# Kernel tuning notes

Measured on AMD Instinct MI355X. Metric: run time of the kernel, lower is better.

The kernel has to match this reference:

```python
import jax, jax.numpy as jnp
import numpy as np

# dims: N nodes, E edges, C channel multiplicity, NS species, RB radial basis, H radial mlp hidden
N, E, C, NS, RB, H = 4000, 128000, 128, 5, 8, 64
AVG_N = 32.0  # avg_n_neighbors


def setup_inputs() -> dict:
    key = jax.random.key(0)
    ks = jax.random.split(key, 17)
    return {
        "x_scalars": jax.random.normal(ks[0], (N, C), jnp.float32),
        "x_vectors": jax.random.normal(ks[1], (N, C, 3), jnp.float32),
        "edge_vectors": jax.random.normal(ks[2], (E, 3), jnp.float32) * 2.0,
        "radial_basis": jax.random.normal(ks[3], (E, RB), jnp.float32),
        "W1_0": jax.random.normal(ks[4], (C, C), jnp.float32),
        "W1_1": jax.random.normal(ks[5], (C, C), jnp.float32),
        "rmlp_w0": jax.random.normal(ks[6], (RB, H), jnp.float32) * np.float32(np.sqrt(4.0 / RB)),
        "rmlp_w1": jax.random.normal(ks[7], (H, H), jnp.float32) * np.float32(np.sqrt(4.0 / H)),
        "rmlp_w2": jax.random.normal(ks[8], (H, H), jnp.float32) * np.float32(np.sqrt(4.0 / H)),
        "rmlp_w3": jax.random.normal(ks[9], (H, 4 * C), jnp.float32) * np.float32(np.sqrt(1.0 / H)),
        "W2_0": jax.random.normal(ks[10], (2 * C, 2 * C), jnp.float32),
        "W2_1": jax.random.normal(ks[11], (2 * C, C), jnp.float32),
        "Wsk0": jax.random.normal(ks[12], (NS, C, 2 * C), jnp.float32),
        "Wsk1": jax.random.normal(ks[13], (NS, C, C), jnp.float32),
        "species": jax.random.randint(ks[14], (N,), 0, NS),
        "senders": jax.random.randint(ks[15], (E,), 0, N),
        "receivers": jax.random.randint(ks[16], (E,), 0, N),
    }


def reference(x_scalars, x_vectors, edge_vectors, radial_basis,
              W1_0, W1_1, rmlp_w0, rmlp_w1, rmlp_w2, rmlp_w3,
              W2_0, W2_1, Wsk0, Wsk1, species, senders, receivers):
    n_nodes = x_scalars.shape[0]
    inv_c = 1.0 / jnp.sqrt(jnp.float32(C))
    # linear_1: per-irrep channel mixing (e3nn path-normalized Linear)
    y0 = (x_scalars @ W1_0) * inv_c                                  # [N,C] 0e
    y1 = jnp.einsum('nci,cd->ndi', x_vectors, W1_1) * inv_c          # [N,C,3] 1o
    # gather to edges
    m0 = y0[senders]                                                 # [E,C]
    m1 = y1[senders]                                                 # [E,C,3]
    # spherical harmonics lmax=1, component normalization: Y0=1, Y1=sqrt(3)*unit_vec
    r = jnp.linalg.norm(edge_vectors, axis=1, keepdims=True)
    u = edge_vectors / jnp.maximum(r, 1e-12)
    Y1 = jnp.sqrt(3.0) * u                                           # [E,3]
    # tensor product filtered to 0e,1o (explicit Clebsch-Gordan, component norm)
    t0a = m0                                                         # 0e x 0e -> 0e
    t0b = jnp.einsum('eci,ei->ec', m1, Y1) / jnp.sqrt(3.0)           # 1o x 1o -> 0e
    t1a = m0[:, :, None] * Y1[:, None, :]                            # 0e x 1o -> 1o
    t1b = m1                                                         # 1o x 0e -> 1o
    # radial MLP (silu, no bias), one scalar weight per tp irrep (4C total)
    h = jax.nn.silu(radial_basis @ rmlp_w0)
    h = jax.nn.silu(h @ rmlp_w1)
    h = jax.nn.silu(h @ rmlp_w2)
    w = h @ rmlp_w3                                                  # [E,4C]
    ws0, ws1 = w[:, :C], w[:, C:2 * C]
    wv0, wv1 = w[:, 2 * C:3 * C], w[:, 3 * C:]
    scal = jnp.concatenate([t0a * ws0, t0b * ws1], axis=1)           # [E,2C]
    vec = jnp.concatenate([t1a * wv0[:, :, None], t1b * wv1[:, :, None]], axis=1)  # [E,2C,3]
    # scatter-add to receivers, neighbor normalization
    inv_nb = 1.0 / jnp.sqrt(jnp.float32(AVG_N))
    agg_s = jax.ops.segment_sum(scal, receivers, num_segments=n_nodes) * inv_nb
    agg_v = jax.ops.segment_sum(vec, receivers, num_segments=n_nodes) * inv_nb
    # linear_2: tp irreps -> (2C)x0e + Cx1o  (C output scalars + C gates)
    inv_2c = 1.0 / jnp.sqrt(jnp.float32(2 * C))
    s = (agg_s @ W2_0) * inv_2c                                      # [N,2C]
    v = jnp.einsum('nci,cd->ndi', agg_v, W2_1) * inv_2c              # [N,C,3]
    # indexed (per-species) skip connection
    s = s + jnp.einsum('nc,ncd->nd', x_scalars, Wsk0[species]) * inv_c
    v = v + jnp.einsum('nci,ncd->ndi', x_vectors, Wsk1[species]) * inv_c
    # gate: silu on scalars, silu(gates) multiplies 1o features
    out_s = jax.nn.silu(s[:, :C])
    gates = jax.nn.silu(s[:, C:])
    out_v = v * gates[:, :, None]
    return jnp.concatenate([out_s, out_v.reshape(n_nodes, 3 * C)], axis=1)  # [N,4C]
```

## Files before the change

kernel.cpp:

```cpp
#include <hip/hip_runtime.h>
#include <math.h>

#define CC 128
#define HH 64
#define RBD 8
#define WDIM 512

typedef __attribute__((ext_vector_type(8))) short short8v;
typedef __attribute__((ext_vector_type(4))) float f32x4;

__device__ __forceinline__ float silu_f(float x) {
    return x / (1.0f + __expf(-x));
}

__device__ __forceinline__ unsigned short f2bf(float x) {
    unsigned int b = __float_as_uint(x);
    unsigned int r = (b + 0x7FFFu + ((b >> 16) & 1u)) >> 16;
    return (unsigned short)r;
}

__device__ __forceinline__ float bf2f(unsigned short u) {
    return __uint_as_float(((unsigned int)u) << 16);
}

__global__ void k_prep(const float* __restrict__ w0, const float* __restrict__ w1,
                       const float* __restrict__ w2, const float* __restrict__ w3,
                       float* __restrict__ w0T, float* __restrict__ w1T,
                       float* __restrict__ w2T, float* __restrict__ w3T,
                       unsigned short* __restrict__ w3bs,
                       unsigned short* __restrict__ w0b,
                       unsigned short* __restrict__ w1b,
                       unsigned short* __restrict__ w2b) {
    int i = blockIdx.x * blockDim.x + threadIdx.x;
    if (i < 64 * 8) { int m = i / 8, k = i % 8; w0T[i] = w0[k * 64 + m]; }
    if (i < 64 * 64) { int m = i / 64, k = i % 64; w1T[i] = w1[k * 64 + m]; w2T[i] = w2[k * 64 + m]; }
    if (i < 512 * 64) { int j = i / 64, k = i % 64; w3T[i] = w3[k * 512 + j]; }
    if (i < 32768) {
        int t = i >> 10, ch = (i >> 9) & 1, lane = (i >> 3) & 63, j = i & 7;
        int k = ch * 32 + 8 * (lane >> 4) + j;
        int n = t * 16 + (lane & 15);
        w3bs[i] = f2bf(w3[k * 512 + n]);
    }
    if (i < 2048) {
        int t = i >> 9, lane = (i >> 3) & 63, j = i & 7;
        int k = 8 * (lane >> 4) + j;
        int col = t * 16 + (lane & 15);
        w0b[i] = (k < RBD) ? f2bf(w0[k * 64 + col]) : (unsigned short)0;
    }
    if (i < 4096) {
        int f = i >> 9, lane = (i >> 3) & 63, j = i & 7;
        int ks = f >> 2, t = f & 3;
        int k = ks * 32 + 8 * (lane >> 4) + j;
        int col = t * 16 + (lane & 15);
        w1b[i] = f2bf(w1[k * 64 + col]);
        w2b[i] = f2bf(w2[k * 64 + col]);
    }
}

__global__ void k_hist(const int* __restrict__ rcv, int* __restrict__ deg, int E_,
                       const int* __restrict__ species, int* __restrict__ scnt, int N) {
    int e = blockIdx.x * blockDim.x + threadIdx.x;
    if (e < E_) atomicAdd(&deg[rcv[e]], 1);
    if (e < N) atomicAdd(&scnt[species[e]], 1);
}

__global__ __launch_bounds__(1024) void k_scan(const int* __restrict__ deg,
                                               int* __restrict__ off, int N,
                                               const int* __restrict__ scnt,
                                               int* __restrict__ soff, int NS) {
    __shared__ int s[1024];
    int t = threadIdx.x;
    int b = t * 4;
    int a0 = (b + 0 < N) ? deg[b + 0] : 0;
    int a1 = (b + 1 < N) ? deg[b + 1] : 0;
    int a2 = (b + 2 < N) ? deg[b + 2] : 0;
    int a3 = (b + 3 < N) ? deg[b + 3] : 0;
    int part = a0 + a1 + a2 + a3;
    s[t] = part;
    __syncthreads();
    for (int d = 1; d < 1024; d <<= 1) {
        int v = (t >= d) ? s[t - d] : 0;
        __syncthreads();
        s[t] += v;
        __syncthreads();
    }
    int excl = s[t] - part;
    if (b + 0 <= N) off[b + 0] = excl;
    if (b + 1 <= N) off[b + 1] = excl + a0;
    if (b + 2 <= N) off[b + 2] = excl + a0 + a1;
    if (b + 3 <= N) off[b + 3] = excl + a0 + a1 + a2;
    if (t == 0) {
        int acc = 0;
        for (int q = 0; q < NS; q++) { soff[q] = acc; acc += scnt[q]; }
        soff[NS] = acc;
    }
}

__global__ void k_scatter(const int* __restrict__ rcv, const int* __restrict__ off,
                          int* __restrict__ cur, int* __restrict__ elist, int E_,
                          const int* __restrict__ species, const int* __restrict__ soff,
                          int* __restrict__ scur, int* __restrict__ nlist, int N) {
    int e = blockIdx.x * blockDim.x + threadIdx.x;
    if (e < E_) {
        int r = rcv[e];
        int p = atomicAdd(&cur[r], 1);
        elist[off[r] + p] = e;
    }
    if (e < N) {
        int s = species[e];
        int p = atomicAdd(&scur[s], 1);
        nlist[soff[s] + p] = e;
    }
}

__global__ __launch_bounds__(128) void k_node_lin(
    const float* __restrict__ xs, const float* __restrict__ xv,
    const float* __restrict__ W10, const float* __restrict__ W11,
    float* __restrict__ y0, float* __restrict__ y1, int N) {
    const int d = threadIdx.x;
    const int n0 = blockIdx.x * 2;
    const int NP = N * CC;
    const float inv_c = 0.08838834764831845f;
    float a0[2] = {0.f, 0.f};
    float av[2][3] = {};
    #pragma unroll 4
    for (int c = 0; c < CC; c++) {
        float w10 = W10[c * CC + d];
        float w11 = W11[c * CC + d];
        #pragma unroll
        for (int n = 0; n < 2; n++) {
            a0[n] += xs[(n0 + n) * CC + c] * w10;
            #pragma unroll
            for (int i = 0; i < 3; i++)
                av[n][i] += xv[((n0 + n) * CC + c) * 3 + i] * w11;
        }
    }
    #pragma unroll
    for (int n = 0; n < 2; n++) {
        y0[(n0 + n) * CC + d] = a0[n] * inv_c;
        #pragma unroll
        for (int i = 0; i < 3; i++)
            y1[i * NP + (n0 + n) * CC + d] = av[n][i] * inv_c;
    }
}

__device__ __forceinline__ void layer64(const float4* a, float4* b,
                                        const float* __restrict__ W) {
    #pragma unroll
    for (int m = 0; m < 16; m++) {
        float s0 = 0.f, s1 = 0.f, s2 = 0.f, s3 = 0.f;
        const float* w0p = W + (4 * m + 0) * 64;
        const float* w1p = W + (4 * m + 1) * 64;
        const float* w2p = W + (4 * m + 2) * 64;
        const float* w3p = W + (4 * m + 3) * 64;
        #pragma unroll
        for (int k = 0; k < 16; k++) {
            float4 av = a[k];
            s0 += av.x * w0p[4 * k + 0] + av.y * w0p[4 * k + 1] + av.z * w0p[4 * k + 2] + av.w * w0p[4 * k + 3];
            s1 += av.x * w1p[4 * k + 0] + av.y * w1p[4 * k + 1] + av.z * w1p[4 * k + 2] + av.w * w1p[4 * k + 3];
            s2 += av.x * w2p[4 * k + 0] + av.y * w2p[4 * k + 1] + av.z * w2p[4 * k + 2] + av.w * w2p[4 * k + 3];
            s3 += av.x * w3p[4 * k + 0] + av.y * w3p[4 * k + 1] + av.z * w3p[4 * k + 2] + av.w * w3p[4 * k + 3];
        }
        b[m] = make_float4(silu_f(s0), silu_f(s1), silu_f(s2), silu_f(s3));
    }
}

__device__ __forceinline__ void mlp_body(
    const float* __restrict__ rb, int e,
    const float* __restrict__ w0T, const float* __restrict__ w1T,
    const float* __restrict__ w2T, float4* a) {
    float rbv[RBD];
    #pragma unroll
    for (int k = 0; k < RBD; k++) rbv[k] = rb[(size_t)e * RBD + k];
    float4 b[16];
    #pragma unroll
    for (int m = 0; m < 16; m++) {
        float s0 = 0.f, s1 = 0.f, s2 = 0.f, s3 = 0.f;
        #pragma unroll
        for (int k = 0; k < RBD; k++) {
            float rv = rbv[k];
            s0 += rv * w0T[(4 * m + 0) * RBD + k];
            s1 += rv * w0T[(4 * m + 1) * RBD + k];
            s2 += rv * w0T[(4 * m + 2) * RBD + k];
            s3 += rv * w0T[(4 * m + 3) * RBD + k];
        }
        a[m] = make_float4(silu_f(s0), silu_f(s1), silu_f(s2), silu_f(s3));
    }
    layer64(a, b, w1T);
    layer64(b, a, w2T);
}

__global__ __launch_bounds__(256) void k_mlpw3(
    const float* __restrict__ rb, const int* __restrict__ elist,
    const int* __restrict__ snd, const float* __restrict__ evec,
    const unsigned short* __restrict__ w0b, const unsigned short* __restrict__ w1b,
    const unsigned short* __restrict__ w2b, const unsigned short* __restrict__ w3bs,
    unsigned int* __restrict__ Wq, float4* __restrict__ up, int* __restrict__ sp,
    int E_) {
    const int lane = threadIdx.x & 63;
    const int wv = threadIdx.x >> 6;
    const int rbk = blockIdx.x * 4 + wv;
    const int col = lane & 15;
    const int grp = lane >> 4;

    if (threadIdx.x < 64) {
        int p = blockIdx.x * 64 + threadIdx.x;
        if (p < E_) {
            int e = elist[p];
            float e0 = evec[(size_t)e * 3 + 0];
            float e1 = evec[(size_t)e * 3 + 1];
            float e2 = evec[(size_t)e * 3 + 2];
            float rn = sqrtf(e0 * e0 + e1 * e1 + e2 * e2);
            float inv = 1.0f / fmaxf(rn, 1e-12f);
            up[p] = make_float4(e0 * inv, e1 * inv, e2 * inv, 0.f);
            sp[p] = snd[e];
        }
    }

    __shared__ unsigned short hbuf[4][16][72];

    short8v a0 = (short8v){0, 0, 0, 0, 0, 0, 0, 0};
    if (grp == 0) {
        int e = elist[rbk * 16 + col];
        const float* rp = rb + (size_t)e * RBD;
        #pragma unroll
        for (int j = 0; j < RBD; j++) a0[j] = (short)f2bf(rp[j]);
    }
    f32x4 acc[4];
    {
        const unsigned short* bp = w0b + (size_t)lane * 8;
        #pragma unroll
        for (int t = 0; t < 4; t++) {
            short8v b = *(const short8v*)(bp + (size_t)t * 512);
            acc[t] = __builtin_amdgcn_mfma_f32_16x16x32_bf16(
                a0, b, (f32x4){0.f, 0.f, 0.f, 0.f}, 0, 0, 0);
        }
    }
    #pragma unroll
    for (int t = 0; t < 4; t++)
        #pragma unroll
        for (int r = 0; r < 4; r++)
            hbuf[wv][grp * 4 + r][t * 16 + col] = f2bf(silu_f(acc[t][r]));

    {
        short8v aA = *(const short8v*)&hbuf[wv][col][8 * grp];
        short8v aB = *(const short8v*)&hbuf[wv][col][32 + 8 * grp];
        const unsigned short* bp = w1b + (size_t)lane * 8;
        #pragma unroll
        for (int t = 0; t < 4; t++) {
            short8v b0 = *(const short8v*)(bp + (size_t)(0 + t) * 512);
            short8v b1 = *(const short8v*)(bp + (size_t)(4 + t) * 512);
            f32x4 c = __builtin_amdgcn_mfma_f32_16x16x32_bf16(
                aA, b0, (f32x4){0.f, 0.f, 0.f, 0.f}, 0, 0, 0);
            acc[t] = __builtin_amdgcn_mfma_f32_16x16x32_bf16(aB, b1, c, 0, 0, 0);
        }
    }
    #pragma unroll
    for (int t = 0; t < 4; t++)
        #pragma unroll
        for (int r = 0; r < 4; r++)
            hbuf[wv][grp * 4 + r][t * 16 + col] = f2bf(silu_f(acc[t][r]));

    {
        short8v aA = *(const short8v*)&hbuf[wv][col][8 * grp];
        short8v aB = *(const short8v*)&hbuf[wv][col][32 + 8 * grp];
        const unsigned short* bp = w2b + (size_t)lane * 8;
        #pragma unroll
        for (int t = 0; t < 4; t++) {
            short8v b0 = *(const short8v*)(bp + (size_t)(0 + t) * 512);
            short8v b1 = *(const short8v*)(bp + (size_t)(4 + t) * 512);
            f32x4 c = __builtin_amdgcn_mfma_f32_16x16x32_bf16(
                aA, b0, (f32x4){0.f, 0.f, 0.f, 0.f}, 0, 0, 0);
            acc[t] = __builtin_amdgcn_mfma_f32_16x16x32_bf16(aB, b1, c, 0, 0, 0);
        }
    }
    #pragma unroll
    for (int t = 0; t < 4; t++)
        #pragma unroll
        for (int r = 0; r < 4; r++)
            hbuf[wv][grp * 4 + r][t * 16 + col] = f2bf(silu_f(acc[t][r]));

    short8v A0 = *(const short8v*)&hbuf[wv][col][8 * grp];
    short8v A1 = *(const short8v*)&hbuf[wv][col][32 + 8 * grp];

    f32x4 wacc[32];
    #pragma unroll
    for (int t = 0; t < 32; t++) wacc[t] = (f32x4){0.f, 0.f, 0.f, 0.f};

    const unsigned short* bbase = w3bs + (size_t)lane * 8;
    #pragma unroll
    for (int t = 0; t < 32; t++) {
        short8v b0 = *(const short8v*)(bbase + (size_t)(t * 2 + 0) * 512);
        short8v b1 = *(const short8v*)(bbase + (size_t)(t * 2 + 1) * 512);
        wacc[t] = __builtin_amdgcn_mfma_f32_16x16x32_bf16(A0, b0, wacc[t], 0, 0, 0);
        wacc[t] = __builtin_amdgcn_mfma_f32_16x16x32_bf16(A1, b1, wacc[t], 0, 0, 0);
    }

    const int rowq = grp * 4;
    const int jbase = rbk * 16 + rowq;
    #pragma unroll
    for (int t = 0; t < 16; t++) {
        #pragma unroll
        for (int rr = 0; rr < 4; rr++) {
            unsigned lo = f2bf(wacc[t][rr]);
            unsigned hi = f2bf(wacc[t + 16][rr]);
            Wq[(size_t)(jbase + rr) * 256 + t * 16 + col] = lo | (hi << 16);
        }
    }
}

__global__ __launch_bounds__(256, 4) void k_gather_em(
    const int* __restrict__ off, const float4* __restrict__ up,
    const int* __restrict__ sp, const unsigned int* __restrict__ Wq,
    const float* __restrict__ y0, const float* __restrict__ y1, int NP,
    float* __restrict__ agg_s, float* __restrict__ agg_v) {
    const int r = blockIdx.x;
    const int tid = threadIdx.x;
    const int half = tid >> 7;
    const int c = tid & 127;
    const int start = off[r];
    const int end = off[r + 1];

    float accs = 0.f, av0 = 0.f, av1 = 0.f, av2 = 0.f;
    const float SQ3 = 1.7320508075688772f;

    auto proc = [&](unsigned wq, float4 u, int s) {
        float wa = bf2f((unsigned short)(wq & 0xFFFFu));
        float wb = bf2f((unsigned short)(wq >> 16));
        if (half == 0) {
            float f = y0[(size_t)s * CC + c];
            accs += f * wa;
            float bb = f * wb * SQ3;
            av0 += bb * u.x; av1 += bb * u.y; av2 += bb * u.z;
        } else {
            float f0 = y1[0 * NP + s * CC + c];
            float f1 = y1[1 * NP + s * CC + c];
            float f2 = y1[2 * NP + s * CC + c];
            accs += (f0 * u.x + f1 * u.y + f2 * u.z) * wa;
            av0 += f0 * wb; av1 += f1 * wb; av2 += f2 * wb;
        }
    };

    int j = start;
    for (; j + 4 <= end; j += 4) {
        unsigned wq0 = Wq[(size_t)(j + 0) * 256 + tid];
        unsigned wq1 = Wq[(size_t)(j + 1) * 256 + tid];
        unsigned wq2 = Wq[(size_t)(j + 2) * 256 + tid];
        unsigned wq3 = Wq[(size_t)(j + 3) * 256 + tid];
        float4 u0 = up[j + 0], u1 = up[j + 1], u2 = up[j + 2], u3 = up[j + 3];
        int s0 = __builtin_amdgcn_readfirstlane(sp[j + 0]);
        int s1 = __builtin_amdgcn_readfirstlane(sp[j + 1]);
        int s2 = __builtin_amdgcn_readfirstlane(sp[j + 2]);
        int s3 = __builtin_amdgcn_readfirstlane(sp[j + 3]);
        proc(wq0, u0, s0);
        proc(wq1, u1, s1);
        proc(wq2, u2, s2);
        proc(wq3, u3, s3);
    }
    for (; j < end; j++) {
        unsigned wq = Wq[(size_t)j * 256 + tid];
        float4 u = up[j];
        int s = __builtin_amdgcn_readfirstlane(sp[j]);
        proc(wq, u, s);
    }

    agg_s[(size_t)r * 256 + tid] = accs;
    float* o = agg_v + ((size_t)r * 256 + tid) * 3;
    o[0] = av0; o[1] = av1; o[2] = av2;
}

__global__ __launch_bounds__(256) void k_mlp_wp(
    const float* __restrict__ rb, const int* __restrict__ elist,
    const float* __restrict__ w0T, const float* __restrict__ w1T,
    const float* __restrict__ w2T, const float* __restrict__ w3T,
    unsigned short* __restrict__ Wp, int E_) {
    int p = blockIdx.x * blockDim.x + threadIdx.x;
    if (p >= E_) return;
    int e = elist[p];
    const int c0 = blockIdx.y * 128;

    float4 a[16];
    mlp_body(rb, e, w0T, w1T, w2T, a);

    const size_t E4 = (size_t)E_ * 4;
    for (int c = c0; c < c0 + 128; c += 8) {
        float s[8];
        #pragma unroll
        for (int q = 0; q < 8; q++) {
            const float* rp = w3T + (size_t)(c + q) * 64;
            float t0 = 0.f, t1 = 0.f, t2 = 0.f, t3 = 0.f;
            #pragma unroll
            for (int k = 0; k < 16; k++) {
                float4 h = a[k];
                t0 += h.x * rp[4 * k + 0];
                t1 += h.y * rp[4 * k + 1];
                t2 += h.z * rp[4 * k + 2];
                t3 += h.w * rp[4 * k + 3];
            }
            s[q] = (t0 + t1) + (t2 + t3);
        }
        ushort4 pk0 = make_ushort4(f2bf(s[0]), f2bf(s[1]), f2bf(s[2]), f2bf(s[3]));
        ushort4 pk1 = make_ushort4(f2bf(s[4]), f2bf(s[5]), f2bf(s[6]), f2bf(s[7]));
        *(ushort4*)(Wp + (size_t)(c >> 2) * E4 + (size_t)p * 4) = pk0;
        *(ushort4*)(Wp + (size_t)((c >> 2) + 1) * E4 + (size_t)p * 4) = pk1;
    }
}

__global__ __launch_bounds__(512, 2) void k_gather_wg(
    const int* __restrict__ off, const int* __restrict__ elist,
    const int* __restrict__ snd, const float* __restrict__ evec,
    const unsigned short* __restrict__ Wp, int E_,
    const float* __restrict__ y0, const float* __restrict__ y1, int NP,
    float* __restrict__ agg_s, float* __restrict__ agg_v) {
    const int r = blockIdx.x;
    const int tid = threadIdx.x;
    const int part = tid >> 7;
    const int c = tid & 127;

    const int start = off[r];
    const int end = off[r + 1];

    const unsigned short* __restrict__ wstream =
        Wp + (size_t)(tid >> 2) * ((size_t)E_ * 4) + (tid & 3);

    float acc0 = 0.f, acc1 = 0.f, acc2 = 0.f;
    const float SQ3 = 1.7320508075688772f;

    #pragma unroll 2
    for (int j = start; j < end; j++) {
        int e = elist[j];
        e = __builtin_amdgcn_readfirstlane(e);
        int s = snd[e];
        s = __builtin_amdgcn_readfirstlane(s);

        float e0 = evec[(size_t)e * 3 + 0];
        float e1 = evec[(size_t)e * 3 + 1];
        float e2 = evec[(size_t)e * 3 + 2];
        float rn = sqrtf(e0 * e0 + e1 * e1 + e2 * e2);
        float inv = 1.0f / fmaxf(rn, 1e-12f);
        float ux = e0 * inv, uy = e1 * inv, uz = e2 * inv;

        float w = bf2f(wstream[(size_t)j * 4]);

        if (part == 0) {
            acc0 += y0[(size_t)s * CC + c] * w;
        } else if (part == 1) {
            float f = y1[0 * NP + s * CC + c] * ux
                    + y1[1 * NP + s * CC + c] * uy
                    + y1[2 * NP + s * CC + c] * uz;
            acc0 += f * w;
        } else if (part == 2) {
            float bb = y0[(size_t)s * CC + c] * w * SQ3;
            acc0 += bb * ux; acc1 += bb * uy; acc2 += bb * uz;
        } else {
            acc0 += y1[0 * NP + s * CC + c] * w;
            acc1 += y1[1 * NP + s * CC + c] * w;
            acc2 += y1[2 * NP + s * CC + c] * w;
        }
    }

    if (part == 0) {
        agg_s[(size_t)r * 256 + c] = acc0;
    } else if (part == 1) {
        agg_s[(size_t)r * 256 + 128 + c] = acc0;
    } else if (part == 2) {
        float* o = agg_v + ((size_t)r * 256 + c) * 3;
        o[0] = acc0; o[1] = acc1; o[2] = acc2;
    } else {
        float* o = agg_v + ((size_t)r * 256 + 128 + c) * 3;
        o[0] = acc0; o[1] = acc1; o[2] = acc2;
    }
}

__global__ void k_mlp(const float* __restrict__ rb,
                      const float* __restrict__ w0T, const float* __restrict__ w1T,
                      const float* __restrict__ w2T,
                      float* __restrict__ h2, int E_) {
    int e = blockIdx.x * blockDim.x + threadIdx.x;
    if (e >= E_) return;
    float4 a[16];
    mlp_body(rb, e, w0T, w1T, w2T, a);
    float4* out = (float4*)(h2 + (size_t)e * HH);
    #pragma unroll
    for (int q = 0; q < 16; q++) out[q] = a[q];
}

__global__ __launch_bounds__(512, 1) void k_gather_h2(
    const int* __restrict__ off, const int* __restrict__ elist,
    const int* __restrict__ snd, const float* __restrict__ evec,
    const float* __restrict__ h2, const float* __restrict__ w3T,
    const float* __restrict__ y0, const float* __restrict__ y1, int NP,
    float* __restrict__ agg_s, float* __restrict__ agg_v) {
    const int r = blockIdx.x;
    const int tid = threadIdx.x;
    const int part = tid >> 7;
    const int c = tid & 127;

    const float4* wp = (const float4*)(w3T + (size_t)tid * 64);
    const int start = off[r];
    const int end = off[r + 1];

    float acc0 = 0.f, acc1 = 0.f, acc2 = 0.f;
    const float SQ3 = 1.7320508075688772f;

    for (int j = start; j < end; j++) {
        int e = elist[j];
        e = __builtin_amdgcn_readfirstlane(e);
        int s = snd[e];
        s = __builtin_amdgcn_readfirstlane(s);

        float e0 = evec[(size_t)e * 3 + 0];
        float e1 = evec[(size_t)e * 3 + 1];
        float e2 = evec[(size_t)e * 3 + 2];
        float rn = sqrtf(e0 * e0 + e1 * e1 + e2 * e2);
        float inv = 1.0f / fmaxf(rn, 1e-12f);
        float ux = e0 * inv, uy = e1 * inv, uz = e2 * inv;

        const float4* __restrict__ hp = (const float4*)(h2 + ((size_t)e << 6));
        float ws0 = 0.f, ws1 = 0.f, ws2 = 0.f, ws3 = 0.f;
        #pragma unroll
        for (int k = 0; k < 16; k++) {
            float4 h = hp[k];
            float4 wv = wp[k];
            ws0 += h.x * wv.x; ws1 += h.y * wv.y; ws2 += h.z * wv.z; ws3 += h.w * wv.w;
        }
        float w = (ws0 + ws1) + (ws2 + ws3);

        if (part == 0) {
            acc0 += y0[(size_t)s * CC + c] * w;
        } else if (part == 1) {
            float f = y1[0 * NP + s * CC + c] * ux
                    + y1[1 * NP + s * CC + c] * uy
                    + y1[2 * NP + s * CC + c] * uz;
            acc0 += f * w;
        } else if (part == 2) {
            float bb = y0[(size_t)s * CC + c] * w * SQ3;
            acc0 += bb * ux; acc1 += bb * uy; acc2 += bb * uz;
        } else {
            acc0 += y1[0 * NP + s * CC + c] * w;
            acc1 += y1[1 * NP + s * CC + c] * w;
            acc2 += y1[2 * NP + s * CC + c] * w;
        }
    }

    if (part == 0) {
        agg_s[(size_t)r * 256 + c] = acc0;
    } else if (part == 1) {
        agg_s[(size_t)r * 256 + 128 + c] = acc0;
    } else if (part == 2) {
        float* o = agg_v + ((size_t)r * 256 + c) * 3;
        o[0] = acc0; o[1] = acc1; o[2] = acc2;
    } else {
        float* o = agg_v + ((size_t)r * 256 + 128 + c) * 3;
        o[0] = acc0; o[1] = acc1; o[2] = acc2;
    }
}

__global__ __launch_bounds__(256) void k_node_out(
    const float* __restrict__ agg_s, const float* __restrict__ agg_v,
    const float* __restrict__ xs, const float* __restrict__ xv,
    const float* __restrict__ W20, const float* __restrict__ W21,
    const float* __restrict__ Wsk0, const float* __restrict__ Wsk1,
    const int* __restrict__ nlist, const int* __restrict__ species,
    float* __restrict__ out, int N) {
    const int tid = threadIdx.x;
    const int b0 = blockIdx.x * 4;
    const int nid0 = nlist[min(b0 + 0, N - 1)];
    const int nid1 = nlist[min(b0 + 1, N - 1)];
    const int nid2 = nlist[min(b0 + 2, N - 1)];
    const int nid3 = nlist[min(b0 + 3, N - 1)];

    __shared__ float as_l[4 * 256];
    __shared__ float av_l[4 * 768];
    __shared__ float xs_l[4 * 128];
    __shared__ float xv_l[4 * 384];
    __shared__ float s_l[4 * 256];

    {
        as_l[0 * 256 + tid] = agg_s[(size_t)nid0 * 256 + tid];
        as_l[1 * 256 + tid] = agg_s[(size_t)nid1 * 256 + tid];
        as_l[2 * 256 + tid] = agg_s[(size_t)nid2 * 256 + tid];
        as_l[3 * 256 + tid] = agg_s[(size_t)nid3 * 256 + tid];
        for (int i = tid; i < 768; i += 256) {
            av_l[0 * 768 + i] = agg_v[(size_t)nid0 * 768 + i];
            av_l[1 * 768 + i] = agg_v[(size_t)nid1 * 768 + i];
            av_l[2 * 768 + i] = agg_v[(size_t)nid2 * 768 + i];
            av_l[3 * 768 + i] = agg_v[(size_t)nid3 * 768 + i];
        }
        if (tid < 128) {
            xs_l[0 * 128 + tid] = xs[(size_t)nid0 * 128 + tid];
            xs_l[1 * 128 + tid] = xs[(size_t)nid1 * 128 + tid];
            xs_l[2 * 128 + tid] = xs[(size_t)nid2 * 128 + tid];
            xs_l[3 * 128 + tid] = xs[(size_t)nid3 * 128 + tid];
        }
        for (int i = tid; i < 384; i += 256) {
            xv_l[0 * 384 + i] = xv[(size_t)nid0 * 384 + i];
            xv_l[1 * 384 + i] = xv[(size_t)nid1 * 384 + i];
            xv_l[2 * 384 + i] = xv[(size_t)nid2 * 384 + i];
            xv_l[3 * 384 + i] = xv[(size_t)nid3 * 384 + i];
        }
    }
    const int sp0 = species[nid0], sp1 = species[nid1];
    const int sp2 = species[nid2], sp3 = species[nid3];
    const bool uni = (sp0 == sp1) && (sp1 == sp2) && (sp2 == sp3);
    __syncthreads();

    const float k_mat = 0.17677669529663687f * 0.0625f;
    const float inv_c = 0.08838834764831845f;

    {
        const int d = tid;
        float am[4] = {0.f, 0.f, 0.f, 0.f};
        for (int cc = 0; cc < 256; cc++) {
            float w = W20[cc * 256 + d];
            #pragma unroll
            for (int n = 0; n < 4; n++) am[n] += as_l[n * 256 + cc] * w;
        }
        float ak[4] = {0.f, 0.f, 0.f, 0.f};
        if (uni) {
            for (int cc = 0; cc < 128; cc++) {
                float w = Wsk0[((size_t)sp0 * 128 + cc) * 256 + d];
                #pragma unroll
                for (int n = 0; n < 4; n++) ak[n] += xs_l[n * 128 + cc] * w;
            }
        } else {
            for (int cc = 0; cc < 128; cc++) {
                float w0v = Wsk0[((size_t)sp0 * 128 + cc) * 256 + d];
                float w1v = Wsk0[((size_t)sp1 * 128 + cc) * 256 + d];
                float w2v = Wsk0[((size_t)sp2 * 128 + cc) * 256 + d];
                float w3v = Wsk0[((size_t)sp3 * 128 + cc) * 256 + d];
                ak[0] += xs_l[0 * 128 + cc] * w0v;
                ak[1] += xs_l[1 * 128 + cc] * w1v;
                ak[2] += xs_l[2 * 128 + cc] * w2v;
                ak[3] += xs_l[3 * 128 + cc] * w3v;
            }
        }
        #pragma unroll
        for (int n = 0; n < 4; n++) s_l[n * 256 + d] = am[n] * k_mat + ak[n] * inv_c;
    }
    __syncthreads();

    if (tid < 128) {
        out[(size_t)nid0 * 512 + tid] = silu_f(s_l[0 * 256 + tid]);
        out[(size_t)nid1 * 512 + tid] = silu_f(s_l[1 * 256 + tid]);
        out[(size_t)nid2 * 512 + tid] = silu_f(s_l[2 * 256 + tid]);
        out[(size_t)nid3 * 512 + tid] = silu_f(s_l[3 * 256 + tid]);
    }

    {
        const int d = tid & 127;
        const int half = tid >> 7;
        const int nA = half ? nid2 : nid0;
        const int nB = half ? nid3 : nid1;
        const int sA = half ? sp2 : sp0;
        const int sB = half ? sp3 : sp1;
        const int la = half ? 2 : 0;
        const int lb = half ? 3 : 1;

        float am[2][3] = {};
        for (int cc = 0; cc < 256; cc++) {
            float w = W21[cc * 128 + d];
            #pragma unroll
            for (int i = 0; i < 3; i++) {
                am[0][i] += av_l[la * 768 + cc * 3 + i] * w;
                am[1][i] += av_l[lb * 768 + cc * 3 + i] * w;
            }
        }
        float ak[2][3] = {};
        if (uni) {
            for (int cc = 0; cc < 128; cc++) {
                float w = Wsk1[((size_t)sp0 * 128 + cc) * 128 + d];
                #pragma unroll
                for (int i = 0; i < 3; i++) {
                    ak[0][i] += xv_l[la * 384 + cc * 3 + i] * w;
                    ak[1][i] += xv_l[lb * 384 + cc * 3 + i] * w;
                }
            }
        } else {
            for (int cc = 0; cc < 128; cc++) {
                float wA = Wsk1[((size_t)sA * 128 + cc) * 128 + d];
                float wB = Wsk1[((size_t)sB * 128 + cc) * 128 + d];
                #pragma unroll
                for (int i = 0; i < 3; i++) {
                    ak[0][i] += xv_l[la * 384 + cc * 3 + i] * wA;
                    ak[1][i] += xv_l[lb * 384 + cc * 3 + i] * wB;
                }
            }
        }
        float gA = silu_f(s_l[la * 256 + 128 + d]);
        float gB = silu_f(s_l[lb * 256 + 128 + d]);
        float* oA = out + (size_t)nA * 512 + 128 + d * 3;
        float* oB = out + (size_t)nB * 512 + 128 + d * 3;
        #pragma unroll
        for (int i = 0; i < 3; i++) {
            oA[i] = (am[0][i] * k_mat + ak[0][i] * inv_c) * gA;
            oB[i] = (am[1][i] * k_mat + ak[1][i] * inv_c) * gB;
        }
    }
}

extern "C" void kernel_launch(void* const* d_in, const int* in_sizes, int n_in,
                              void* d_out, int out_size, void* d_ws, size_t ws_size,
                              hipStream_t stream) {
    const float* xs   = (const float*)d_in[0];
    const float* xv   = (const float*)d_in[1];
    const float* evec = (const float*)d_in[2];
    const float* rb   = (const float*)d_in[3];
    const float* W10  = (const float*)d_in[4];
    const float* W11  = (const float*)d_in[5];
    const float* w0   = (const float*)d_in[6];
    const float* w1   = (const float*)d_in[7];
    const float* w2   = (const float*)d_in[8];
    const float* w3   = (const float*)d_in[9];
    const float* W20  = (const float*)d_in[10];
    const float* W21  = (const float*)d_in[11];
    const float* Wsk0 = (const float*)d_in[12];
    const float* Wsk1 = (const float*)d_in[13];
    const int* species = (const int*)d_in[14];
    const int* snd = (const int*)d_in[15];
    const int* rcv = (const int*)d_in[16];

    const int N = in_sizes[0] / CC;
    const int E = in_sizes[2] / 3;
    const int NP = N * CC;
    int NS = in_sizes[12] / (CC * 2 * CC);
    if (NS < 1) NS = 1;
    if (NS > 63) NS = 63;

    float* ws   = (float*)d_ws;
    float* y0   = ws;
    float* y1   = y0 + (size_t)N * CC;
    float* aggs = y1 + (size_t)N * CC * 3;
    float* aggv = aggs + (size_t)N * 2 * CC;
    float* w0T  = aggv + (size_t)N * 2 * CC * 3;
    float* w1T  = w0T + 64 * 8;
    float* w2T  = w1T + 64 * 64;
    float* w3T  = w2T + 64 * 64;
    unsigned short* w3bs = (unsigned short*)(w3T + 512 * 64);
    unsigned short* w0b  = w3bs + 32768;
    unsigned short* w1b  = w0b + 2048;
    unsigned short* w2b  = w1b + 4096;
    int*   deg  = (int*)(w2b + 4096);
    int*   cur  = deg + 4096;
    int*   scnt = cur + 4096;
    int*   soff = scnt + 64;
    int*   scur = soff + 72;
    int*   off  = scur + 64;
    int*   elist = off + 4160;
    float4* up  = (float4*)(elist + E);
    int*   sp   = (int*)(up + E);
    int*   nlist = sp + E;
    void*  big  = (void*)(nlist + N);

    size_t base_bytes = (size_t)((char*)big - (char*)d_ws);
    size_t wq_bytes   = (size_t)E * 256 * sizeof(unsigned int);
    size_t need_A = base_bytes + wq_bytes;
    size_t need_B = base_bytes + (size_t)E * WDIM * sizeof(unsigned short);

    unsigned int*   Wq  = (unsigned int*)big;
    unsigned short* Wp  = (unsigned short*)big;

    hipMemsetAsync(deg, 0, (4096 + 4096 + 64 + 72 + 64) * sizeof(int), stream);
    hipLaunchKernelGGL(k_hist, dim3((E + 255) / 256), dim3(256), 0, stream,
                       rcv, deg, E, species, scnt, N);
    hipLaunchKernelGGL(k_scan, dim3(1), dim3(1024), 0, stream,
                       deg, off, N, scnt, soff, NS);
    hipLaunchKernelGGL(k_scatter, dim3((E + 255) / 256), dim3(256), 0, stream,
                       rcv, off, cur, elist, E, species, soff, scur, nlist, N);
    hipLaunchKernelGGL(k_prep, dim3(128), dim3(256), 0, stream,
                       w0, w1, w2, w3, w0T, w1T, w2T, w3T, w3bs, w0b, w1b, w2b);
    hipLaunchKernelGGL(k_node_lin, dim3(N / 2), dim3(128), 0, stream,
                       xs, xv, W10, W11, y0, y1, N);

    if (ws_size >= need_A && (E % 64) == 0) {
        hipLaunchKernelGGL(k_mlpw3, dim3(E / 64), dim3(256), 0, stream,
                           rb, elist, snd, evec, w0b, w1b, w2b, w3bs, Wq, up, sp, E);
        hipLaunchKernelGGL(k_gather_em, dim3(N), dim3(256), 0, stream,
                           off, up, sp, Wq, y0, y1, NP, aggs, aggv);
    } else if (ws_size >= need_B) {
        hipLaunchKernelGGL(k_mlp_wp, dim3((E + 255) / 256, 4), dim3(256), 0, stream,
                           rb, elist, w0T, w1T, w2T, w3T, Wp, E);
        hipLaunchKernelGGL(k_gather_wg, dim3(N), dim3(512), 0, stream,
                           off, elist, snd, evec, Wp, E, y0, y1, NP, aggs, aggv);
    } else {
        hipLaunchKernelGGL(k_mlp, dim3((E + 255) / 256), dim3(256), 0, stream,
                           rb, w0T, w1T, w2T, (float*)big, E);
        hipLaunchKernelGGL(k_gather_h2, dim3(N), dim3(512), 0, stream,
                           off, elist, snd, evec, (const float*)big, w3T,
                           y0, y1, NP, aggs, aggv);
    }

    hipLaunchKernelGGL(k_node_out, dim3((N + 3) / 4), dim3(256), 0, stream,
                       aggs, aggv, xs, xv, W20, W21, Wsk0, Wsk1, nlist, species,
                       (float*)d_out, N);
}
```

Measured before the change: 287.3 us.

## Fuse weight prep into histogram and node linear into edge MLP launch

Merges the weight-prep kernel into the receiver histogram kernel and appends node-linear blocks to the edge MLP kernel grid, removing two launches and letting node_lin overlap with MLP work. The node_lin kernel is also restructured to stage the node inputs in shared memory and use 256 threads, one node per half-block. This trades launch overhead and serial gaps for larger shared memory use in the MLP kernel and mixed block types within one grid.

```diff
diff --git a/kernel.cpp b/kernel.cpp
--- a/kernel.cpp
+++ b/kernel.cpp
@@ -23,15 +23,19 @@
     return __uint_as_float(((unsigned int)u) << 16);
 }
 
-__global__ void k_prep(const float* __restrict__ w0, const float* __restrict__ w1,
-                       const float* __restrict__ w2, const float* __restrict__ w3,
-                       float* __restrict__ w0T, float* __restrict__ w1T,
-                       float* __restrict__ w2T, float* __restrict__ w3T,
-                       unsigned short* __restrict__ w3bs,
-                       unsigned short* __restrict__ w0b,
-                       unsigned short* __restrict__ w1b,
-                       unsigned short* __restrict__ w2b) {
+__global__ void k_prep_hist(const float* __restrict__ w0, const float* __restrict__ w1,
+                            const float* __restrict__ w2, const float* __restrict__ w3,
+                            float* __restrict__ w0T, float* __restrict__ w1T,
+                            float* __restrict__ w2T, float* __restrict__ w3T,
+                            unsigned short* __restrict__ w3bs,
+                            unsigned short* __restrict__ w0b,
+                            unsigned short* __restrict__ w1b,
+                            unsigned short* __restrict__ w2b,
+                            const int* __restrict__ rcv, int* __restrict__ deg, int E_,
+                            const int* __restrict__ species, int* __restrict__ scnt, int N) {
     int i = blockIdx.x * blockDim.x + threadIdx.x;
+    if (i < E_) atomicAdd(&deg[rcv[i]], 1);
+    if (i < N) atomicAdd(&scnt[species[i]], 1);
     if (i < 64 * 8) { int m = i / 8, k = i % 8; w0T[i] = w0[k * 64 + m]; }
     if (i < 64 * 64) { int m = i / 64, k = i % 64; w1T[i] = w1[k * 64 + m]; w2T[i] = w2[k * 64 + m]; }
     if (i < 512 * 64) { int j = i / 64, k = i % 64; w3T[i] = w3[k * 512 + j]; }
@@ -55,13 +59,6 @@
         w1b[i] = f2bf(w1[k * 64 + col]);
         w2b[i] = f2bf(w2[k * 64 + col]);
     }
-}
-
-__global__ void k_hist(const int* __restrict__ rcv, int* __restrict__ deg, int E_,
-                       const int* __restrict__ species, int* __restrict__ scnt, int N) {
-    int e = blockIdx.x * blockDim.x + threadIdx.x;
-    if (e < E_) atomicAdd(&deg[rcv[e]], 1);
-    if (e < N) atomicAdd(&scnt[species[e]], 1);
 }
 
 __global__ __launch_bounds__(1024) void k_scan(const int* __restrict__ deg,
@@ -113,35 +110,38 @@
     }
 }
 
-__global__ __launch_bounds__(128) void k_node_lin(
+__global__ __launch_bounds__(256) void k_node_lin(
     const float* __restrict__ xs, const float* __restrict__ xv,
     const float* __restrict__ W10, const float* __restrict__ W11,
     float* __restrict__ y0, float* __restrict__ y1, int N) {
-    const int d = threadIdx.x;
+    const int tid = threadIdx.x;
     const int n0 = blockIdx.x * 2;
     const int NP = N * CC;
+    const int d = tid & 127;
+    const int nn = tid >> 7;
     const float inv_c = 0.08838834764831845f;
-    float a0[2] = {0.f, 0.f};
-    float av[2][3] = {};
+
+    __shared__ float xsl[2][128];
+    __shared__ float xvl[2][384];
+    if (tid < 256) xsl[tid >> 7][tid & 127] = xs[(size_t)n0 * 128 + tid];
+    for (int i = tid; i < 768; i += 256) xvl[i / 384][i % 384] = xv[(size_t)n0 * 384 + i];
+    __syncthreads();
+
+    float a0 = 0.f, av0 = 0.f, av1 = 0.f, av2 = 0.f;
     #pragma unroll 4
     for (int c = 0; c < CC; c++) {
         float w10 = W10[c * CC + d];
         float w11 = W11[c * CC + d];
-        #pragma unroll
-        for (int n = 0; n < 2; n++) {
-            a0[n] += xs[(n0 + n) * CC + c] * w10;
-            #pragma unroll
-            for (int i = 0; i < 3; i++)
-                av[n][i] += xv[((n0 + n) * CC + c) * 3 + i] * w11;
-        }
-    }
-    #pragma unroll
-    for (int n = 0; n < 2; n++) {
-        y0[(n0 + n) * CC + d] = a0[n] * inv_c;
-        #pragma unroll
-        for (int i = 0; i < 3; i++)
-            y1[i * NP + (n0 + n) * CC + d] = av[n][i] * inv_c;
-    }
+        float xsv = xsl[nn][c];
+        a0 += xsv * w10;
+        av0 += xvl[nn][c * 3 + 0] * w11;
+        av1 += xvl[nn][c * 3 + 1] * w11;
+        av2 += xvl[nn][c * 3 + 2] * w11;
+    }
+    y0[(size_t)(n0 + nn) * CC + d] = a0 * inv_c;
+    y1[0 * NP + (size_t)(n0 + nn) * CC + d] = av0 * inv_c;
+    y1[1 * NP + (size_t)(n0 + nn) * CC + d] = av1 * inv_c;
+    y1[2 * NP + (size_t)(n0 + nn) * CC + d] = av2 * inv_c;
 }
 
 __device__ __forceinline__ void layer64(const float4* a, float4* b,
@@ -196,7 +196,43 @@
     const unsigned short* __restrict__ w0b, const unsigned short* __restrict__ w1b,
     const unsigned short* __restrict__ w2b, const unsigned short* __restrict__ w3bs,
     unsigned int* __restrict__ Wq, float4* __restrict__ up, int* __restrict__ sp,
-    int E_) {
+    int E_, int nblk_mlp,
+    const float* __restrict__ xs, const float* __restrict__ xv,
+    const float* __restrict__ W10, const float* __restrict__ W11,
+    float* __restrict__ y0, float* __restrict__ y1, int NP) {
+    __shared__ unsigned short hbuf[4][16][72];
+    __shared__ float xsl[2][128];
+    __shared__ float xvl[2][384];
+
+    if (blockIdx.x >= nblk_mlp) {
+        const int tid = threadIdx.x;
+        const int n0 = (blockIdx.x - nblk_mlp) * 2;
+        const int d = tid & 127;
+        const int nn = tid >> 7;
+        const float inv_c = 0.08838834764831845f;
+
+        xsl[tid >> 7][tid & 127] = xs[(size_t)n0 * 128 + tid];
+        for (int i = tid; i < 768; i += 256) xvl[i / 384][i % 384] = xv[(size_t)n0 * 384 + i];
+        __syncthreads();
+
+        float a0 = 0.f, av0 = 0.f, av1 = 0.f, av2 = 0.f;
+        #pragma unroll 4
+        for (int c = 0; c < CC; c++) {
+            float w10 = W10[c * CC + d];
+            float w11 = W11[c * CC + d];
+            float xsv = xsl[nn][c];
+            a0 += xsv * w10;
+            av0 += xvl[nn][c * 3 + 0] * w11;
+            av1 += xvl[nn][c * 3 + 1] * w11;
+            av2 += xvl[nn][c * 3 + 2] * w11;
+        }
+        y0[(size_t)(n0 + nn) * CC + d] = a0 * inv_c;
+        y1[0 * NP + (size_t)(n0 + nn) * CC + d] = av0 * inv_c;
+        y1[1 * NP + (size_t)(n0 + nn) * CC + d] = av1 * inv_c;
+        y1[2 * NP + (size_t)(n0 + nn) * CC + d] = av2 * inv_c;
+        return;
+    }
+
     const int lane = threadIdx.x & 63;
     const int wv = threadIdx.x >> 6;
     const int rbk = blockIdx.x * 4 + wv;
@@ -216,8 +252,6 @@
             sp[p] = snd[e];
         }
     }
-
-    __shared__ unsigned short hbuf[4][16][72];
 
     short8v a0 = (short8v){0, 0, 0, 0, 0, 0, 0, 0};
     if (grp == 0) {
@@ -761,28 +795,31 @@
     unsigned short* Wp  = (unsigned short*)big;
 
     hipMemsetAsync(deg, 0, (4096 + 4096 + 64 + 72 + 64) * sizeof(int), stream);
-    hipLaunchKernelGGL(k_hist, dim3((E + 255) / 256), dim3(256), 0, stream,
+    hipLaunchKernelGGL(k_prep_hist, dim3((E + 255) / 256), dim3(256), 0, stream,
+                       w0, w1, w2, w3, w0T, w1T, w2T, w3T, w3bs, w0b, w1b, w2b,
                        rcv, deg, E, species, scnt, N);
     hipLaunchKernelGGL(k_scan, dim3(1), dim3(1024), 0, stream,
                        deg, off, N, scnt, soff, NS);
     hipLaunchKernelGGL(k_scatter, dim3((E + 255) / 256), dim3(256), 0, stream,
                        rcv, off, cur, elist, E, species, soff, scur, nlist, N);
-    hipLaunchKernelGGL(k_prep, dim3(128), dim3(256), 0, stream,
-                       w0, w1, w2, w3, w0T, w1T, w2T, w3T, w3bs, w0b, w1b, w2b);
-    hipLaunchKernelGGL(k_node_lin, dim3(N / 2), dim3(128), 0, stream,
-                       xs, xv, W10, W11, y0, y1, N);
-
-    if (ws_size >= need_A && (E % 64) == 0) {
-        hipLaunchKernelGGL(k_mlpw3, dim3(E / 64), dim3(256), 0, stream,
-                           rb, elist, snd, evec, w0b, w1b, w2b, w3bs, Wq, up, sp, E);
+
+    if (ws_size >= need_A && (E % 64) == 0 && (N % 2) == 0) {
+        const int nblk_mlp = E / 64;
+        hipLaunchKernelGGL(k_mlpw3, dim3(nblk_mlp + N / 2), dim3(256), 0, stream,
+                           rb, elist, snd, evec, w0b, w1b, w2b, w3bs, Wq, up, sp,
+                           E, nblk_mlp, xs, xv, W10, W11, y0, y1, NP);
         hipLaunchKernelGGL(k_gather_em, dim3(N), dim3(256), 0, stream,
                            off, up, sp, Wq, y0, y1, NP, aggs, aggv);
     } else if (ws_size >= need_B) {
+        hipLaunchKernelGGL(k_node_lin, dim3((N + 1) / 2), dim3(256), 0, stream,
+                           xs, xv, W10, W11, y0, y1, N);
         hipLaunchKernelGGL(k_mlp_wp, dim3((E + 255) / 256, 4), dim3(256), 0, stream,
                            rb, elist, w0T, w1T, w2T, w3T, Wp, E);
         hipLaunchKernelGGL(k_gather_wg, dim3(N), dim3(512), 0, stream,
                            off, elist, snd, evec, Wp, E, y0, y1, NP, aggs, aggv);
     } else {
+        hipLaunchKernelGGL(k_node_lin, dim3((N + 1) / 2), dim3(256), 0, stream,
+                           xs, xv, W10, W11, y0, y1, N);
         hipLaunchKernelGGL(k_mlp, dim3((E + 255) / 256), dim3(256), 0, stream,
                            rb, w0T, w1T, w2T, (float*)big, E);
         hipLaunchKernelGGL(k_gather_h2, dim3(N), dim3(512), 0, stream,
```

New measurement: 272.8 us. 1.05x faster.
